# Kernel tuning notes

Hardware: AMD Instinct MI355X
Metric: run time of the kernel (lower is better)

Reference implementation:

```python
import jax, jax.numpy as jnp
import numpy as np

N_CLASSES = 80
IMAGE_SIZE = 608
IGNORE_THR = 0.5
MAX_BOXES = 128  # fixed-size padded replacement for torch's data-dependent masked_select
BATCH = 8
GRIDS = (19, 38, 76)
ANCHORS_NP = np.array([[10, 13], [16, 30], [33, 23], [30, 61], [62, 45], [59, 119],
                       [116, 90], [156, 198], [373, 326]], dtype=np.float32)


def setup_inputs() -> dict:
    key = jax.random.key(0)
    out = {}
    for i, G in enumerate(GRIDS):
        kf, k1, k2, k3, k4 = jax.random.split(jax.random.fold_in(key, i), 5)
        out[f"feature_map_{i}"] = 0.5 * jax.random.normal(kf, (BATCH, 3 * (5 + N_CLASSES), G, G), jnp.float32)
        xy = jax.random.uniform(k1, (BATCH, G, G, 3, 2), jnp.float32, 0.0, float(IMAGE_SIZE))
        wh = jax.random.uniform(k2, (BATCH, G, G, 3, 2), jnp.float32, 10.0, 300.0)
        obj = jax.random.bernoulli(k3, 0.003, (BATCH, G, G, 3, 1)).astype(jnp.float32)
        cls = jax.nn.one_hot(jax.random.randint(k4, (BATCH, G, G, 3), 0, N_CLASSES), N_CLASSES, dtype=jnp.float32)
        out[f"y_true_{i}"] = jnp.concatenate([xy * obj, wh * obj, obj, cls * obj], axis=-1)
    out["anchors"] = jnp.asarray(ANCHORS_NP)
    return out


def _bce_logits(logits, targets):
    # binary_cross_entropy_with_logits, elementwise, numerically stable
    return jnp.maximum(logits, 0.0) - logits * targets + jax.nn.softplus(-jnp.abs(logits))


def _predict_transform(fm, anchors3):
    B, _, G, _ = fm.shape
    stride = IMAGE_SIZE // G
    attrs = 5 + N_CLASSES
    p = fm.reshape(B, 3 * attrs, G * G).transpose(0, 2, 1).reshape(B, G, G, 3, attrs)
    xy, wh, conf, prob = jnp.split(p, [2, 4, 5], axis=-1)
    gx, gy = jnp.meshgrid(jnp.arange(G), jnp.arange(G))  # 'xy' indexing: gx[i,j]=j, gy[i,j]=i
    offset = jnp.stack([gx, gy], axis=-1).astype(p.dtype)[:, :, None, :]  # [G,G,1,2]
    centers = (jax.nn.sigmoid(xy) + offset) * stride  # [B,G,G,3,2]
    sizes = jnp.exp(wh) * (anchors3 / stride) * stride
    boxes = jnp.concatenate([centers, sizes], axis=-1)  # [B,G,G,3,4]
    return offset, boxes, conf, prob, stride


def _ignore_mask(boxes, y_true):
    # Vectorized version of the per-batch masked_select loop: gather up to
    # MAX_BOXES GT boxes per image via top_k on the object flag, mask padding.
    B = boxes.shape[0]
    flags = y_true[..., 4].reshape(B, -1)          # [B, G*G*3]
    tb = y_true[..., :4].reshape(B, -1, 4)          # [B, G*G*3, 4]
    vals, idx = jax.lax.top_k(flags, MAX_BOXES)     # [B,K]
    sel = jnp.take_along_axis(tb, idx[..., None], axis=1)  # [B,K,4]
    valid = vals > 0.5                              # [B,K]
    pxy = boxes[..., 0:2][..., None, :]             # [B,G,G,3,1,2]
    pwh = boxes[..., 2:4][..., None, :]
    txy = sel[:, None, None, None, :, 0:2]          # [B,1,1,1,K,2]
    twh = sel[:, None, None, None, :, 2:4]
    mins = jnp.maximum(pxy - pwh * 0.5, txy - twh * 0.5)
    maxs = jnp.minimum(pxy + pwh * 0.5, txy + twh * 0.5)
    iwh = jnp.maximum(maxs - mins, 0.0)
    inter = iwh[..., 0] * iwh[..., 1]               # [B,G,G,3,K]
    pa = pwh[..., 0] * pwh[..., 1]
    ta = twh[..., 0] * twh[..., 1]
    iou = inter / (pa + ta - inter + 1e-10)
    iou = jnp.where(valid[:, None, None, None, :], iou, 0.0)
    best = jnp.max(iou, axis=-1)                    # [B,G,G,3]
    return (best <= IGNORE_THR).astype(boxes.dtype)[..., None]  # [B,G,G,3,1]


def _scale_loss(fm, yt, anchors3):
    B = yt.shape[0]
    offset, boxes, conf_logits, prob_logits, stride = _predict_transform(fm, anchors3)
    obj = yt[..., 4:5]
    ign = _ignore_mask(boxes, yt)
    pred_xy = boxes[..., 0:2] / stride - offset
    true_xy = yt[..., 0:2] / stride - offset
    true_tw = yt[..., 2:4] / anchors3
    pred_tw = boxes[..., 2:4] / anchors3
    true_tw = jnp.where(true_tw == 0, 1.0, true_tw)
    pred_tw = jnp.where(pred_tw == 0, 1.0, pred_tw)
    true_tw = jnp.log(jnp.clip(true_tw, 1e-9, 1e9))
    pred_tw = jnp.log(jnp.clip(pred_tw, 1e-9, 1e9))
    box_scale = 2.0 - (yt[..., 2:3] / IMAGE_SIZE) * (yt[..., 3:4] / IMAGE_SIZE)
    xy_loss = jnp.sum(5.0 * obj * box_scale * (pred_xy - true_xy) ** 2) / B
    wh_loss = jnp.sum(5.0 * obj * box_scale * (pred_tw - true_tw) ** 2) / B
    bce = _bce_logits(conf_logits, obj)
    conf = obj * bce + 0.5 * (1.0 - obj) * ign * bce
    focal = jnp.abs(obj - jax.nn.sigmoid(conf_logits)) ** 2  # alpha=1, gamma=2
    conf_loss = jnp.sum(conf * focal) / B
    delta = 0.01
    tgt = (1.0 - delta) * yt[..., 5:] + delta / N_CLASSES
    class_loss = jnp.sum(obj * _bce_logits(prob_logits, tgt)) / B
    return xy_loss, wh_loss, conf_loss, class_loss


def reference(feature_map_0, feature_map_1, feature_map_2, y_true_0, y_true_1, y_true_2, anchors):
    fms = (feature_map_0, feature_map_1, feature_map_2)
    yts = (y_true_0, y_true_1, y_true_2)
    list_anchors = (anchors[6:9], anchors[3:6], anchors[0:3])
    xy = wh = cf = pb = 0.0
    for fm, yt, a3 in zip(fms, yts, list_anchors):
        l_xy, l_wh, l_cf, l_pb = _scale_loss(fm, yt, a3)
        xy = xy + l_xy; wh = wh + l_wh; cf = cf + l_cf; pb = pb + l_pb
    total = xy + wh + cf + pb
    return (total, xy, wh, cf, pb)
```

## Files before the change

kernel.cpp:

```cpp
#include <hip/hip_runtime.h>
#include <math.h>

#define NCLS   80
#define ATTRS  85
#define BATCH  8
#define MAXB   128
#define CHCAP  64

constexpr int G0 = 19, G1 = 38, G2 = 76;
constexpr int S0 = G0 * G0, S1 = G1 * G1, S2 = G2 * G2;
constexpr int NPOS0 = 3 * S0, NPOS1 = 3 * S1, NPOS2 = 3 * S2;
constexpr int NCH0 = (NPOS0 + 255) / 256;
constexpr int NCH1 = (NPOS1 + 255) / 256;
constexpr int NCH2 = (NPOS2 + 255) / 256;
constexpr int CHB1 = NCH0 * BATCH;
constexpr int CHB2 = CHB1 + NCH1 * BATCH;
constexpr int TOTCH = CHB2 + NCH2 * BATCH;
constexpr int BW0 = (NPOS0 + 31) / 32;
constexpr int BW1 = (NPOS1 + 31) / 32;
constexpr int BW2 = (NPOS2 + 31) / 32;
constexpr int BMB0 = 0, BMB1 = BW0 * BATCH, BMB2 = BMB1 + BW1 * BATCH;
#define CPB 128
constexpr int MC0 = (S0 + CPB - 1) / CPB;
constexpr int MC1 = (S1 + CPB - 1) / CPB;
constexpr int MC2 = (S2 + CPB - 1) / CPB;
constexpr int MB0 = BATCH * 3 * MC0, MB1 = BATCH * 3 * MC1, MB2 = BATCH * 3 * MC2;
constexpr int NMAIN = MB0 + MB1 + MB2;

#define OFF_CHUNKCNT 0
#define OFF_CHUNKBOX 4096
#define OFF_BITMAP   (4096 + 737280)
#define OFF_PARTA    (4096 + 737280 + 22912)
#define OFF_PARTC    (4096 + 737280 + 22912 + 11520)

__global__ __launch_bounds__(256) void collectA(
    const float* __restrict__ yt0, const float* __restrict__ yt1, const float* __restrict__ yt2,
    const float* __restrict__ fm0, const float* __restrict__ fm1, const float* __restrict__ fm2,
    const float* __restrict__ anchors,
    float4* __restrict__ chunkbox, int* __restrict__ chunkcnt,
    unsigned* __restrict__ bitmap, float* __restrict__ partA)
{
    int blk = blockIdx.x;
    const float* yt; const float* fm;
    int b, c, npos, s, Sv, G, aoff; float strd;
    if (blk < CHB1)      { int q = blk;        b = q / NCH0; c = q % NCH0; npos = NPOS0; yt = yt0; fm = fm0; s = 0; Sv = S0; G = G0; strd = 32.f; aoff = 12; }
    else if (blk < CHB2) { int q = blk - CHB1; b = q / NCH1; c = q % NCH1; npos = NPOS1; yt = yt1; fm = fm1; s = 1; Sv = S1; G = G1; strd = 16.f; aoff = 6; }
    else                 { int q = blk - CHB2; b = q / NCH2; c = q % NCH2; npos = NPOS2; yt = yt2; fm = fm2; s = 2; Sv = S2; G = G2; strd = 8.f;  aoff = 0; }

    int tid = threadIdx.x, wv = tid >> 6, lane = tid & 63;
    int r = c * 256 + tid;
    bool f = false; size_t off = 0;
    if (r < npos) { off = ((size_t)b * npos + r) * ATTRS; f = (yt[off + 4] > 0.5f); }
    unsigned long long m = __ballot(f);

    __shared__ unsigned long long bal[4];
    __shared__ int pr[CHCAP];
    __shared__ float4 pbox[CHCAP];
    __shared__ float wred[4][3];
    if (lane == 0) bal[wv] = m;
    __syncthreads();

    int nw    = (s == 0) ? BW0 : ((s == 1) ? BW1 : BW2);
    int wbase = ((s == 0) ? BMB0 : ((s == 1) ? BMB1 : BMB2)) + b * nw;
    if (tid < 8) {
        int widx = c * 8 + tid;
        if (widx < nw) {
            unsigned long long bm = bal[tid >> 1];
            bitmap[wbase + widx] = (tid & 1) ? (unsigned)(bm >> 32) : (unsigned)bm;
        }
    }

    int prefix = 0, tot = 0;
    #pragma unroll
    for (int i = 0; i < 4; ++i) { int pc = __popcll(bal[i]); if (i < wv) prefix += pc; tot += pc; }
    int myp = prefix + __popcll(m & ((1ull << lane) - 1ull));

    if (f && myp < CHCAP) {
        float4 v; v.x = yt[off]; v.y = yt[off + 1]; v.z = yt[off + 2]; v.w = yt[off + 3];
        chunkbox[blk * CHCAP + myp] = v;
        pr[myp] = r; pbox[myp] = v;
    }
    if (tid == 0) chunkcnt[blk] = (tot > CHCAP) ? CHCAP : tot;
    __syncthreads();

    int np = (tot > CHCAP) ? CHCAP : tot;
    float axy = 0.f, awh = 0.f, acl = 0.f;
    for (int p = wv; p < np; p += 4) {
        int rp = pr[p]; float4 bx = pbox[p];
        int pos = rp / 3, a = rp - pos * 3;
        size_t fb = ((size_t)(b * 255 + a * 85)) * Sv + pos;
        size_t yb = ((size_t)b * npos + rp) * ATTRS;
        float term;
        {
            float pl  = fm[fb + (size_t)(5 + lane) * Sv];
            float tv  = yt[yb + 5 + lane];
            float tgt = 0.99f * tv + 1.25e-4f;
            term = fmaxf(pl, 0.f) - pl * tgt + __logf(1.f + __expf(-fabsf(pl)));
        }
        if (lane < 16) {
            int cc = 64 + lane;
            float pl  = fm[fb + (size_t)(5 + cc) * Sv];
            float tv  = yt[yb + 5 + cc];
            float tgt = 0.99f * tv + 1.25e-4f;
            term += fmaxf(pl, 0.f) - pl * tgt + __logf(1.f + __expf(-fabsf(pl)));
        }
        #pragma unroll
        for (int o = 32; o > 0; o >>= 1) term += __shfl_down(term, o);
        if (lane == 0) {
            float tx = fm[fb];
            float ty = fm[fb + (size_t)Sv];
            float tw = fm[fb + 2 * (size_t)Sv];
            float th = fm[fb + 3 * (size_t)Sv];
            int yr = pos / G, xc = pos - yr * G;
            float sx = 1.f / (1.f + __expf(-tx));
            float sy = 1.f / (1.f + __expf(-ty));
            float predx = (sx + (float)xc) - (float)xc;
            float predy = (sy + (float)yr) - (float)yr;
            float truex = bx.x / strd - (float)xc;
            float truey = bx.y / strd - (float)yr;
            float bs = 2.f - (bx.z / 608.f) * (bx.w / 608.f);
            float dx = predx - truex, dy = predy - truey;
            axy += 5.f * bs * (dx * dx + dy * dy);
            float aw = anchors[aoff + a * 2], ah = anchors[aoff + a * 2 + 1];
            float ttw = __logf(bx.z / aw), tth = __logf(bx.w / ah);
            float dw = tw - ttw, dh = th - tth;
            awh += 5.f * bs * (dw * dw + dh * dh);
            acl += term;
        }
    }
    if (lane == 0) { wred[wv][0] = axy; wred[wv][1] = awh; wred[wv][2] = acl; }
    __syncthreads();
    if (tid == 0) {
        partA[blk * 4 + 0] = wred[0][0] + wred[1][0] + wred[2][0] + wred[3][0];
        partA[blk * 4 + 1] = wred[0][1] + wred[1][1] + wred[2][1] + wred[3][1];
        partA[blk * 4 + 2] = wred[0][2] + wred[1][2] + wred[2][2] + wred[3][2];
        partA[blk * 4 + 3] = 0.f;
    }
}

__global__ __launch_bounds__(128) void conf_final_k(
    const float* __restrict__ fm0, const float* __restrict__ fm1, const float* __restrict__ fm2,
    const float* __restrict__ anchors,
    const float4* __restrict__ chunkbox, const int* __restrict__ chunkcnt,
    const unsigned* __restrict__ bitmap,
    const float4* __restrict__ partA, float* __restrict__ partC,
    float* __restrict__ out)
{
    int blk = blockIdx.x, tid = threadIdx.x;
    int wv = tid >> 6, lane = tid & 63;

    if (blk < NMAIN) {
        int s, q, nchk, G, Sv, aoff; const float* fm; float strd;
        if (blk < MB0)            { s = 0; q = blk;             nchk = MC0; G = G0; Sv = S0; fm = fm0; strd = 32.f; aoff = 12; }
        else if (blk < MB0 + MB1) { s = 1; q = blk - MB0;       nchk = MC1; G = G1; Sv = S1; fm = fm1; strd = 16.f; aoff = 6; }
        else                      { s = 2; q = blk - MB0 - MB1; nchk = MC2; G = G2; Sv = S2; fm = fm2; strd = 8.f;  aoff = 0; }
        int b = q / (3 * nchk); int rem = q % (3 * nchk); int a = rem / nchk; int c = rem % nchk;

        __shared__ float4 sbox[MAXB];
        __shared__ int    cs[130], ps[130];
        __shared__ int    tot_s;
        __shared__ float  sred[2];

        int pos = c * CPB + tid;
        int vld = (pos < Sv);
        size_t fb = ((size_t)(b * 255 + a * 85)) * Sv + (vld ? pos : 0);
        float tx = fm[fb];
        float ty = fm[fb + (size_t)Sv];
        float tw = fm[fb + 2 * (size_t)Sv];
        float th = fm[fb + 3 * (size_t)Sv];
        float tc = fm[fb + 4 * (size_t)Sv];

        int base = (s == 0) ? (b * NCH0) : ((s == 1) ? (CHB1 + b * NCH1) : (CHB2 + b * NCH2));
        int nch  = (s == 0) ? NCH0 : ((s == 1) ? NCH1 : NCH2);
        cs[tid] = (tid < nch) ? chunkcnt[base + tid] : 0;
        __syncthreads();

        if (wv == 0) {
            int c0 = cs[2 * lane], c1 = cs[2 * lane + 1];
            int v = c0 + c1;
            #pragma unroll
            for (int o = 1; o < 64; o <<= 1) {
                int t = __shfl_up(v, o);
                if (lane >= o) v += t;
            }
            int excl = v - (c0 + c1);
            ps[2 * lane]     = excl;
            ps[2 * lane + 1] = excl + c0;
            if (lane == 63) tot_s = v;
        }
        __syncthreads();
        int tot = tot_s;
        int cnt = (tot > MAXB) ? MAXB : tot;

        if (tid < cnt) {
            int lo = 0, hi = nch - 1;
            while (lo < hi) {
                int mid = (lo + hi + 1) >> 1;
                if (ps[mid] <= tid) lo = mid; else hi = mid - 1;
            }
            int j = tid - ps[lo];
            float4 v = chunkbox[(size_t)(base + lo) * CHCAP + j];
            float hw = 0.5f * v.z, hh = 0.5f * v.w;
            sbox[tid] = make_float4(v.x - hw, v.y - hh, v.x + hw, v.y + hh);
        }
        __syncthreads();

        float acc = 0.f;
        if (vld) {
            float aw = anchors[aoff + a * 2], ah = anchors[aoff + a * 2 + 1];
            int yr = pos / G, xc = pos - yr * G;
            float sxg = 1.f / (1.f + __expf(-tx));
            float syg = 1.f / (1.f + __expf(-ty));
            float cx = (sxg + (float)xc) * strd;
            float cy = (syg + (float)yr) * strd;
            float pw = __expf(tw) * aw;
            float ph = __expf(th) * ah;

            int rr = pos * 3 + a;
            int nw    = (s == 0) ? BW0 : ((s == 1) ? BW1 : BW2);
            int wbase = ((s == 0) ? BMB0 : ((s == 1) ? BMB1 : BMB2)) + b * nw;
            unsigned wd = bitmap[wbase + (rr >> 5)];
            float obj = ((wd >> (rr & 31)) & 1u) ? 1.f : 0.f;

            float pa = pw * ph;
            float px0 = cx - 0.5f * pw, py0 = cy - 0.5f * ph;
            float px1 = cx + 0.5f * pw, py1 = cy + 0.5f * ph;
            float best = -1.f;
            for (int j = 0; j < cnt; ++j) {
                float4 bb = sbox[j];
                float ix0 = fmaxf(px0, bb.x);
                float iy0 = fmaxf(py0, bb.y);
                float ix1 = fminf(px1, bb.z);
                float iy1 = fminf(py1, bb.w);
                float iw = fmaxf(ix1 - ix0, 0.f);
                float ih = fmaxf(iy1 - iy0, 0.f);
                float ta = (bb.z - bb.x) * (bb.w - bb.y);
                best = fmaxf(best, 3.f * (iw * ih) - (pa + ta));
            }
            float ign = (best <= 0.f) ? 1.f : 0.f;

            float e    = __expf(-fabsf(tc));
            float l1pe = __logf(1.f + e);
            float bce  = fmaxf(tc, 0.f) - tc * obj + l1pe;
            float sg   = (tc >= 0.f) ? (1.f / (1.f + e)) : (e / (1.f + e));
            float df   = fabsf(obj - sg);
            acc = (obj * bce + 0.5f * (1.f - obj) * ign * bce) * (df * df);
        }

        #pragma unroll
        for (int o = 32; o > 0; o >>= 1) acc += __shfl_down(acc, o);
        if (lane == 0) sred[wv] = acc;
        __syncthreads();
        if (tid == 0) {
            __hip_atomic_store(&partC[blk], sred[0] + sred[1],
                               __ATOMIC_RELAXED, __HIP_MEMORY_SCOPE_AGENT);
        }
    } else {
        float xy = 0.f, wh = 0.f, cl = 0.f;
        for (int i = tid; i < TOTCH; i += 128) {
            float4 v = partA[i];
            xy += v.x; wh += v.y; cl += v.z;
        }
        float cf = 0.f;
        for (int i = tid; i < NMAIN; i += 128) {
            float v; int it = 0;
            do {
                v = __hip_atomic_load(&partC[i], __ATOMIC_RELAXED, __HIP_MEMORY_SCOPE_AGENT);
                if (v > 0.f) break;
                __builtin_amdgcn_s_sleep(2);
            } while (++it < (1 << 18));
            cf += (v > 0.f) ? v : 0.f;
        }
        #pragma unroll
        for (int o = 32; o > 0; o >>= 1) {
            xy += __shfl_down(xy, o);
            wh += __shfl_down(wh, o);
            cl += __shfl_down(cl, o);
            cf += __shfl_down(cf, o);
        }
        __shared__ float red[2][4];
        if (lane == 0) { red[wv][0] = xy; red[wv][1] = wh; red[wv][2] = cl; red[wv][3] = cf; }
        __syncthreads();
        if (tid == 0) {
            float X = (red[0][0] + red[1][0]) * 0.125f;
            float W = (red[0][1] + red[1][1]) * 0.125f;
            float P = (red[0][2] + red[1][2]) * 0.125f;
            float C = (red[0][3] + red[1][3]) * 0.125f;
            out[0] = X + W + C + P;
            out[1] = X; out[2] = W; out[3] = C; out[4] = P;
        }
    }
}

extern "C" void kernel_launch(void* const* d_in, const int* in_sizes, int n_in,
                              void* d_out, int out_size, void* d_ws, size_t ws_size,
                              hipStream_t stream) {
    const float* fm0 = (const float*)d_in[0];
    const float* yt0 = (const float*)d_in[1];
    const float* fm1 = (const float*)d_in[2];
    const float* yt1 = (const float*)d_in[3];
    const float* fm2 = (const float*)d_in[4];
    const float* yt2 = (const float*)d_in[5];
    const float* anch = (const float*)d_in[6];

    char* ws = (char*)d_ws;
    int*      chunkcnt = (int*)(ws + OFF_CHUNKCNT);
    float4*   chunkbox = (float4*)(ws + OFF_CHUNKBOX);
    unsigned* bitmap   = (unsigned*)(ws + OFF_BITMAP);
    float*    partA    = (float*)(ws + OFF_PARTA);
    float*    partC    = (float*)(ws + OFF_PARTC);

    collectA<<<TOTCH, 256, 0, stream>>>(yt0, yt1, yt2, fm0, fm1, fm2, anch,
                                        chunkbox, chunkcnt, bitmap, partA);
    conf_final_k<<<NMAIN + 1, 128, 0, stream>>>(fm0, fm1, fm2, anch,
                                                chunkbox, chunkcnt, bitmap,
                                                (const float4*)partA, partC, (float*)d_out);
}
```

Measured before the change: 23.29 us.

## Fuse collect and conf kernels into one launch with flag-based inter-block polling

Result: slower. 83.46 us (+258.3%).

```diff
diff --git a/kernel.cpp b/kernel.cpp
--- a/kernel.cpp
+++ b/kernel.cpp
@@ -6,6 +6,7 @@
 #define BATCH  8
 #define MAXB   128
 #define CHCAP  64
+#define POLL_TIMEOUT (1 << 18)
 
 constexpr int G0 = 19, G1 = 38, G2 = 76;
 constexpr int S0 = G0 * G0, S1 = G1 * G1, S2 = G2 * G2;
@@ -20,12 +21,10 @@
 constexpr int BW1 = (NPOS1 + 31) / 32;
 constexpr int BW2 = (NPOS2 + 31) / 32;
 constexpr int BMB0 = 0, BMB1 = BW0 * BATCH, BMB2 = BMB1 + BW1 * BATCH;
-#define CPB 128
-constexpr int MC0 = (S0 + CPB - 1) / CPB;
-constexpr int MC1 = (S1 + CPB - 1) / CPB;
-constexpr int MC2 = (S2 + CPB - 1) / CPB;
+constexpr int MC0 = (S0 + 255) / 256, MC1 = (S1 + 255) / 256, MC2 = (S2 + 255) / 256;
 constexpr int MB0 = BATCH * 3 * MC0, MB1 = BATCH * 3 * MC1, MB2 = BATCH * 3 * MC2;
 constexpr int NMAIN = MB0 + MB1 + MB2;
+constexpr int NBLK_TOT = TOTCH + NMAIN + 1;
 
 #define OFF_CHUNKCNT 0
 #define OFF_CHUNKBOX 4096
@@ -33,135 +32,131 @@
 #define OFF_PARTA    (4096 + 737280 + 22912)
 #define OFF_PARTC    (4096 + 737280 + 22912 + 11520)
 
-__global__ __launch_bounds__(256) void collectA(
+__global__ __launch_bounds__(256, 6) void fused_k(
     const float* __restrict__ yt0, const float* __restrict__ yt1, const float* __restrict__ yt2,
     const float* __restrict__ fm0, const float* __restrict__ fm1, const float* __restrict__ fm2,
     const float* __restrict__ anchors,
     float4* __restrict__ chunkbox, int* __restrict__ chunkcnt,
-    unsigned* __restrict__ bitmap, float* __restrict__ partA)
-{
-    int blk = blockIdx.x;
-    const float* yt; const float* fm;
-    int b, c, npos, s, Sv, G, aoff; float strd;
-    if (blk < CHB1)      { int q = blk;        b = q / NCH0; c = q % NCH0; npos = NPOS0; yt = yt0; fm = fm0; s = 0; Sv = S0; G = G0; strd = 32.f; aoff = 12; }
-    else if (blk < CHB2) { int q = blk - CHB1; b = q / NCH1; c = q % NCH1; npos = NPOS1; yt = yt1; fm = fm1; s = 1; Sv = S1; G = G1; strd = 16.f; aoff = 6; }
-    else                 { int q = blk - CHB2; b = q / NCH2; c = q % NCH2; npos = NPOS2; yt = yt2; fm = fm2; s = 2; Sv = S2; G = G2; strd = 8.f;  aoff = 0; }
-
-    int tid = threadIdx.x, wv = tid >> 6, lane = tid & 63;
-    int r = c * 256 + tid;
-    bool f = false; size_t off = 0;
-    if (r < npos) { off = ((size_t)b * npos + r) * ATTRS; f = (yt[off + 4] > 0.5f); }
-    unsigned long long m = __ballot(f);
-
-    __shared__ unsigned long long bal[4];
-    __shared__ int pr[CHCAP];
-    __shared__ float4 pbox[CHCAP];
-    __shared__ float wred[4][3];
-    if (lane == 0) bal[wv] = m;
-    __syncthreads();
-
-    int nw    = (s == 0) ? BW0 : ((s == 1) ? BW1 : BW2);
-    int wbase = ((s == 0) ? BMB0 : ((s == 1) ? BMB1 : BMB2)) + b * nw;
-    if (tid < 8) {
-        int widx = c * 8 + tid;
-        if (widx < nw) {
-            unsigned long long bm = bal[tid >> 1];
-            bitmap[wbase + widx] = (tid & 1) ? (unsigned)(bm >> 32) : (unsigned)bm;
-        }
-    }
-
-    int prefix = 0, tot = 0;
-    #pragma unroll
-    for (int i = 0; i < 4; ++i) { int pc = __popcll(bal[i]); if (i < wv) prefix += pc; tot += pc; }
-    int myp = prefix + __popcll(m & ((1ull << lane) - 1ull));
-
-    if (f && myp < CHCAP) {
-        float4 v; v.x = yt[off]; v.y = yt[off + 1]; v.z = yt[off + 2]; v.w = yt[off + 3];
-        chunkbox[blk * CHCAP + myp] = v;
-        pr[myp] = r; pbox[myp] = v;
-    }
-    if (tid == 0) chunkcnt[blk] = (tot > CHCAP) ? CHCAP : tot;
-    __syncthreads();
-
-    int np = (tot > CHCAP) ? CHCAP : tot;
-    float axy = 0.f, awh = 0.f, acl = 0.f;
-    for (int p = wv; p < np; p += 4) {
-        int rp = pr[p]; float4 bx = pbox[p];
-        int pos = rp / 3, a = rp - pos * 3;
-        size_t fb = ((size_t)(b * 255 + a * 85)) * Sv + pos;
-        size_t yb = ((size_t)b * npos + rp) * ATTRS;
-        float term;
-        {
-            float pl  = fm[fb + (size_t)(5 + lane) * Sv];
-            float tv  = yt[yb + 5 + lane];
-            float tgt = 0.99f * tv + 1.25e-4f;
-            term = fmaxf(pl, 0.f) - pl * tgt + __logf(1.f + __expf(-fabsf(pl)));
-        }
-        if (lane < 16) {
-            int cc = 64 + lane;
-            float pl  = fm[fb + (size_t)(5 + cc) * Sv];
-            float tv  = yt[yb + 5 + cc];
-            float tgt = 0.99f * tv + 1.25e-4f;
-            term += fmaxf(pl, 0.f) - pl * tgt + __logf(1.f + __expf(-fabsf(pl)));
-        }
-        #pragma unroll
-        for (int o = 32; o > 0; o >>= 1) term += __shfl_down(term, o);
-        if (lane == 0) {
-            float tx = fm[fb];
-            float ty = fm[fb + (size_t)Sv];
-            float tw = fm[fb + 2 * (size_t)Sv];
-            float th = fm[fb + 3 * (size_t)Sv];
-            int yr = pos / G, xc = pos - yr * G;
-            float sx = 1.f / (1.f + __expf(-tx));
-            float sy = 1.f / (1.f + __expf(-ty));
-            float predx = (sx + (float)xc) - (float)xc;
-            float predy = (sy + (float)yr) - (float)yr;
-            float truex = bx.x / strd - (float)xc;
-            float truey = bx.y / strd - (float)yr;
-            float bs = 2.f - (bx.z / 608.f) * (bx.w / 608.f);
-            float dx = predx - truex, dy = predy - truey;
-            axy += 5.f * bs * (dx * dx + dy * dy);
-            float aw = anchors[aoff + a * 2], ah = anchors[aoff + a * 2 + 1];
-            float ttw = __logf(bx.z / aw), tth = __logf(bx.w / ah);
-            float dw = tw - ttw, dh = th - tth;
-            awh += 5.f * bs * (dw * dw + dh * dh);
-            acl += term;
-        }
-    }
-    if (lane == 0) { wred[wv][0] = axy; wred[wv][1] = awh; wred[wv][2] = acl; }
-    __syncthreads();
-    if (tid == 0) {
-        partA[blk * 4 + 0] = wred[0][0] + wred[1][0] + wred[2][0] + wred[3][0];
-        partA[blk * 4 + 1] = wred[0][1] + wred[1][1] + wred[2][1] + wred[3][1];
-        partA[blk * 4 + 2] = wred[0][2] + wred[1][2] + wred[2][2] + wred[3][2];
-        partA[blk * 4 + 3] = 0.f;
-    }
-}
-
-__global__ __launch_bounds__(128) void conf_final_k(
-    const float* __restrict__ fm0, const float* __restrict__ fm1, const float* __restrict__ fm2,
-    const float* __restrict__ anchors,
-    const float4* __restrict__ chunkbox, const int* __restrict__ chunkcnt,
-    const unsigned* __restrict__ bitmap,
-    const float4* __restrict__ partA, float* __restrict__ partC,
+    unsigned* __restrict__ bitmap,
+    float* __restrict__ partA, float* __restrict__ partC,
     float* __restrict__ out)
 {
-    int blk = blockIdx.x, tid = threadIdx.x;
-    int wv = tid >> 6, lane = tid & 63;
-
-    if (blk < NMAIN) {
+    int blk = blockIdx.x, tid = threadIdx.x, wv = tid >> 6, lane = tid & 63;
+
+    if (blk < TOTCH) {
+        const float* yt; const float* fm;
+        int b, c, npos, s, Sv, G, aoff; float strd;
+        if (blk < CHB1)      { int q = blk;        b = q / NCH0; c = q % NCH0; npos = NPOS0; yt = yt0; fm = fm0; s = 0; Sv = S0; G = G0; strd = 32.f; aoff = 12; }
+        else if (blk < CHB2) { int q = blk - CHB1; b = q / NCH1; c = q % NCH1; npos = NPOS1; yt = yt1; fm = fm1; s = 1; Sv = S1; G = G1; strd = 16.f; aoff = 6; }
+        else                 { int q = blk - CHB2; b = q / NCH2; c = q % NCH2; npos = NPOS2; yt = yt2; fm = fm2; s = 2; Sv = S2; G = G2; strd = 8.f;  aoff = 0; }
+
+        int r = c * 256 + tid;
+        bool f = false; size_t off = 0;
+        if (r < npos) { off = ((size_t)b * npos + r) * ATTRS; f = (yt[off + 4] > 0.5f); }
+        unsigned long long m = __ballot(f);
+
+        __shared__ unsigned long long bal[4];
+        __shared__ int pr[CHCAP];
+        __shared__ float4 pbox[CHCAP];
+        __shared__ float wred[4][3];
+        if (lane == 0) bal[wv] = m;
+        __syncthreads();
+
+        int nw    = (s == 0) ? BW0 : ((s == 1) ? BW1 : BW2);
+        int wbase = ((s == 0) ? BMB0 : ((s == 1) ? BMB1 : BMB2)) + b * nw;
+        if (tid < 8) {
+            int widx = c * 8 + tid;
+            if (widx < nw) {
+                unsigned long long bm = bal[tid >> 1];
+                bitmap[wbase + widx] = (tid & 1) ? (unsigned)(bm >> 32) : (unsigned)bm;
+            }
+        }
+
+        int prefix = 0, tot = 0;
+        #pragma unroll
+        for (int i = 0; i < 4; ++i) { int pc = __popcll(bal[i]); if (i < wv) prefix += pc; tot += pc; }
+        int myp = prefix + __popcll(m & ((1ull << lane) - 1ull));
+
+        if (f && myp < CHCAP) {
+            float4 v; v.x = yt[off]; v.y = yt[off + 1]; v.z = yt[off + 2]; v.w = yt[off + 3];
+            chunkbox[blk * CHCAP + myp] = v;
+            pr[myp] = r; pbox[myp] = v;
+        }
+        __syncthreads();
+
+        int np = (tot > CHCAP) ? CHCAP : tot;
+        if (tid == 0) {
+            __hip_atomic_store(&chunkcnt[blk], np + 1, __ATOMIC_RELEASE, __HIP_MEMORY_SCOPE_AGENT);
+        }
+
+        float axy = 0.f, awh = 0.f, acl = 0.f;
+        for (int p = wv; p < np; p += 4) {
+            int rp = pr[p]; float4 bx = pbox[p];
+            int pos = rp / 3, a = rp - pos * 3;
+            size_t fb = ((size_t)(b * 255 + a * 85)) * Sv + pos;
+            size_t yb = ((size_t)b * npos + rp) * ATTRS;
+            float term;
+            {
+                float pl  = fm[fb + (size_t)(5 + lane) * Sv];
+                float tv  = yt[yb + 5 + lane];
+                float tgt = 0.99f * tv + 1.25e-4f;
+                term = fmaxf(pl, 0.f) - pl * tgt + __logf(1.f + __expf(-fabsf(pl)));
+            }
+            if (lane < 16) {
+                int cc = 64 + lane;
+                float pl  = fm[fb + (size_t)(5 + cc) * Sv];
+                float tv  = yt[yb + 5 + cc];
+                float tgt = 0.99f * tv + 1.25e-4f;
+                term += fmaxf(pl, 0.f) - pl * tgt + __logf(1.f + __expf(-fabsf(pl)));
+            }
+            #pragma unroll
+            for (int o = 32; o > 0; o >>= 1) term += __shfl_down(term, o);
+            if (lane == 0) {
+                float tx = fm[fb];
+                float ty = fm[fb + (size_t)Sv];
+                float tw = fm[fb + 2 * (size_t)Sv];
+                float th = fm[fb + 3 * (size_t)Sv];
+                int yr = pos / G, xc = pos - yr * G;
+                float sx = 1.f / (1.f + __expf(-tx));
+                float sy = 1.f / (1.f + __expf(-ty));
+                float predx = (sx + (float)xc) - (float)xc;
+                float predy = (sy + (float)yr) - (float)yr;
+                float truex = bx.x / strd - (float)xc;
+                float truey = bx.y / strd - (float)yr;
+                float bs = 2.f - (bx.z / 608.f) * (bx.w / 608.f);
+                float dx = predx - truex, dy = predy - truey;
+                axy += 5.f * bs * (dx * dx + dy * dy);
+                float aw = anchors[aoff + a * 2], ah = anchors[aoff + a * 2 + 1];
+                float ttw = __logf(bx.z / aw), tth = __logf(bx.w / ah);
+                float dw = tw - ttw, dh = th - tth;
+                awh += 5.f * bs * (dw * dw + dh * dh);
+                acl += term;
+            }
+        }
+        if (lane == 0) { wred[wv][0] = axy; wred[wv][1] = awh; wred[wv][2] = acl; }
+        __syncthreads();
+        if (tid == 0) {
+            float4* pav = (float4*)partA;
+            pav[blk] = make_float4(wred[0][0] + wred[1][0] + wred[2][0] + wred[3][0],
+                                   wred[0][1] + wred[1][1] + wred[2][1] + wred[3][1],
+                                   wred[0][2] + wred[1][2] + wred[2][2] + wred[3][2], 0.f);
+            __hip_atomic_store(&partA[blk * 4 + 3], 1.0f, __ATOMIC_RELEASE, __HIP_MEMORY_SCOPE_AGENT);
+        }
+
+    } else if (blk < TOTCH + NMAIN) {
+        int u = blk - TOTCH;
         int s, q, nchk, G, Sv, aoff; const float* fm; float strd;
-        if (blk < MB0)            { s = 0; q = blk;             nchk = MC0; G = G0; Sv = S0; fm = fm0; strd = 32.f; aoff = 12; }
-        else if (blk < MB0 + MB1) { s = 1; q = blk - MB0;       nchk = MC1; G = G1; Sv = S1; fm = fm1; strd = 16.f; aoff = 6; }
-        else                      { s = 2; q = blk - MB0 - MB1; nchk = MC2; G = G2; Sv = S2; fm = fm2; strd = 8.f;  aoff = 0; }
+        if (u < MB0)            { s = 0; q = u;             nchk = MC0; G = G0; Sv = S0; fm = fm0; strd = 32.f; aoff = 12; }
+        else if (u < MB0 + MB1) { s = 1; q = u - MB0;       nchk = MC1; G = G1; Sv = S1; fm = fm1; strd = 16.f; aoff = 6; }
+        else                    { s = 2; q = u - MB0 - MB1; nchk = MC2; G = G2; Sv = S2; fm = fm2; strd = 8.f;  aoff = 0; }
         int b = q / (3 * nchk); int rem = q % (3 * nchk); int a = rem / nchk; int c = rem % nchk;
 
         __shared__ float4 sbox[MAXB];
         __shared__ int    cs[130], ps[130];
         __shared__ int    tot_s;
-        __shared__ float  sred[2];
-
-        int pos = c * CPB + tid;
+        __shared__ float  sred[4];
+
+        int pos = c * 256 + tid;
         int vld = (pos < Sv);
         size_t fb = ((size_t)(b * 255 + a * 85)) * Sv + (vld ? pos : 0);
         float tx = fm[fb];
@@ -172,8 +167,20 @@
 
         int base = (s == 0) ? (b * NCH0) : ((s == 1) ? (CHB1 + b * NCH1) : (CHB2 + b * NCH2));
         int nch  = (s == 0) ? NCH0 : ((s == 1) ? NCH1 : NCH2);
-        cs[tid] = (tid < nch) ? chunkcnt[base + tid] : 0;
-        __syncthreads();
+        if (tid < 128) {
+            int v1 = 0;
+            if (tid < nch) {
+                int it = 0;
+                do {
+                    v1 = __hip_atomic_load(&chunkcnt[base + tid], __ATOMIC_RELAXED, __HIP_MEMORY_SCOPE_AGENT);
+                    if (v1 > 0) break;
+                    __builtin_amdgcn_s_sleep(2);
+                } while (++it < POLL_TIMEOUT);
+            }
+            cs[tid] = (v1 > 0) ? (v1 - 1) : 0;
+        }
+        __syncthreads();
+        __threadfence();
 
         if (wv == 0) {
             int c0 = cs[2 * lane], c1 = cs[2 * lane + 1];
@@ -252,23 +259,36 @@
         if (lane == 0) sred[wv] = acc;
         __syncthreads();
         if (tid == 0) {
-            __hip_atomic_store(&partC[blk], sred[0] + sred[1],
+            __hip_atomic_store(&partC[u], sred[0] + sred[1] + sred[2] + sred[3],
                                __ATOMIC_RELAXED, __HIP_MEMORY_SCOPE_AGENT);
         }
+
     } else {
+        for (int i = tid; i < TOTCH; i += 256) {
+            int it = 0;
+            while (it < POLL_TIMEOUT) {
+                float v = __hip_atomic_load(&partA[i * 4 + 3], __ATOMIC_RELAXED, __HIP_MEMORY_SCOPE_AGENT);
+                if (v == 1.0f) break;
+                __builtin_amdgcn_s_sleep(2);
+                ++it;
+            }
+        }
+        __syncthreads();
+        __threadfence();
         float xy = 0.f, wh = 0.f, cl = 0.f;
-        for (int i = tid; i < TOTCH; i += 128) {
-            float4 v = partA[i];
+        const float4* pav = (const float4*)partA;
+        for (int i = tid; i < TOTCH; i += 256) {
+            float4 v = pav[i];
             xy += v.x; wh += v.y; cl += v.z;
         }
         float cf = 0.f;
-        for (int i = tid; i < NMAIN; i += 128) {
+        for (int i = tid; i < NMAIN; i += 256) {
             float v; int it = 0;
             do {
                 v = __hip_atomic_load(&partC[i], __ATOMIC_RELAXED, __HIP_MEMORY_SCOPE_AGENT);
                 if (v > 0.f) break;
                 __builtin_amdgcn_s_sleep(2);
-            } while (++it < (1 << 18));
+            } while (++it < POLL_TIMEOUT);
             cf += (v > 0.f) ? v : 0.f;
         }
         #pragma unroll
@@ -278,14 +298,14 @@
             cl += __shfl_down(cl, o);
             cf += __shfl_down(cf, o);
         }
-        __shared__ float red[2][4];
+        __shared__ float red[4][4];
         if (lane == 0) { red[wv][0] = xy; red[wv][1] = wh; red[wv][2] = cl; red[wv][3] = cf; }
         __syncthreads();
         if (tid == 0) {
-            float X = (red[0][0] + red[1][0]) * 0.125f;
-            float W = (red[0][1] + red[1][1]) * 0.125f;
-            float P = (red[0][2] + red[1][2]) * 0.125f;
-            float C = (red[0][3] + red[1][3]) * 0.125f;
+            float X = (red[0][0] + red[1][0] + red[2][0] + red[3][0]) * 0.125f;
+            float W = (red[0][1] + red[1][1] + red[2][1] + red[3][1]) * 0.125f;
+            float P = (red[0][2] + red[1][2] + red[2][2] + red[3][2]) * 0.125f;
+            float C = (red[0][3] + red[1][3] + red[2][3] + red[3][3]) * 0.125f;
             out[0] = X + W + C + P;
             out[1] = X; out[2] = W; out[3] = C; out[4] = P;
         }
@@ -310,9 +330,7 @@
     float*    partA    = (float*)(ws + OFF_PARTA);
     float*    partC    = (float*)(ws + OFF_PARTC);
 
-    collectA<<<TOTCH, 256, 0, stream>>>(yt0, yt1, yt2, fm0, fm1, fm2, anch,
-                                        chunkbox, chunkcnt, bitmap, partA);
-    conf_final_k<<<NMAIN + 1, 128, 0, stream>>>(fm0, fm1, fm2, anch,
-                                                chunkbox, chunkcnt, bitmap,
-                                                (const float4*)partA, partC, (float*)d_out);
+    fused_k<<<NBLK_TOT, 256, 0, stream>>>(yt0, yt1, yt2, fm0, fm1, fm2, anch,
+                                          chunkbox, chunkcnt, bitmap,
+                                          partA, partC, (float*)d_out);
 }
```

## Move positive-box loss work from collect kernel into second kernel blocks

Applied to the files above, without the earlier changes.

Result: slower. 31.03 us (+33.2%).

```diff
diff --git a/kernel.cpp b/kernel.cpp
--- a/kernel.cpp
+++ b/kernel.cpp
@@ -6,6 +6,7 @@
 #define BATCH  8
 #define MAXB   128
 #define CHCAP  64
+#define POLL_TIMEOUT (1 << 18)
 
 constexpr int G0 = 19, G1 = 38, G2 = 76;
 constexpr int S0 = G0 * G0, S1 = G1 * G1, S2 = G2 * G2;
@@ -26,26 +27,26 @@
 constexpr int MC2 = (S2 + CPB - 1) / CPB;
 constexpr int MB0 = BATCH * 3 * MC0, MB1 = BATCH * 3 * MC1, MB2 = BATCH * 3 * MC2;
 constexpr int NMAIN = MB0 + MB1 + MB2;
+constexpr int NBLK2 = NMAIN + TOTCH + 1;
 
 #define OFF_CHUNKCNT 0
 #define OFF_CHUNKBOX 4096
-#define OFF_BITMAP   (4096 + 737280)
-#define OFF_PARTA    (4096 + 737280 + 22912)
-#define OFF_PARTC    (4096 + 737280 + 22912 + 11520)
+#define OFF_CHUNKIDX (4096 + 737280)
+#define OFF_BITMAP   (4096 + 737280 + 184320)
+#define OFF_PARTA    (4096 + 737280 + 184320 + 22912)
+#define OFF_PARTC    (4096 + 737280 + 184320 + 22912 + 11520)
 
 __global__ __launch_bounds__(256) void collectA(
     const float* __restrict__ yt0, const float* __restrict__ yt1, const float* __restrict__ yt2,
-    const float* __restrict__ fm0, const float* __restrict__ fm1, const float* __restrict__ fm2,
-    const float* __restrict__ anchors,
-    float4* __restrict__ chunkbox, int* __restrict__ chunkcnt,
-    unsigned* __restrict__ bitmap, float* __restrict__ partA)
+    float4* __restrict__ chunkbox, int* __restrict__ chunkidx, int* __restrict__ chunkcnt,
+    unsigned* __restrict__ bitmap)
 {
     int blk = blockIdx.x;
-    const float* yt; const float* fm;
-    int b, c, npos, s, Sv, G, aoff; float strd;
-    if (blk < CHB1)      { int q = blk;        b = q / NCH0; c = q % NCH0; npos = NPOS0; yt = yt0; fm = fm0; s = 0; Sv = S0; G = G0; strd = 32.f; aoff = 12; }
-    else if (blk < CHB2) { int q = blk - CHB1; b = q / NCH1; c = q % NCH1; npos = NPOS1; yt = yt1; fm = fm1; s = 1; Sv = S1; G = G1; strd = 16.f; aoff = 6; }
-    else                 { int q = blk - CHB2; b = q / NCH2; c = q % NCH2; npos = NPOS2; yt = yt2; fm = fm2; s = 2; Sv = S2; G = G2; strd = 8.f;  aoff = 0; }
+    const float* yt;
+    int b, c, npos, s;
+    if (blk < CHB1)      { int q = blk;        b = q / NCH0; c = q % NCH0; npos = NPOS0; yt = yt0; s = 0; }
+    else if (blk < CHB2) { int q = blk - CHB1; b = q / NCH1; c = q % NCH1; npos = NPOS1; yt = yt1; s = 1; }
+    else                 { int q = blk - CHB2; b = q / NCH2; c = q % NCH2; npos = NPOS2; yt = yt2; s = 2; }
 
     int tid = threadIdx.x, wv = tid >> 6, lane = tid & 63;
     int r = c * 256 + tid;
@@ -54,9 +55,6 @@
     unsigned long long m = __ballot(f);
 
     __shared__ unsigned long long bal[4];
-    __shared__ int pr[CHCAP];
-    __shared__ float4 pbox[CHCAP];
-    __shared__ float wred[4][3];
     if (lane == 0) bal[wv] = m;
     __syncthreads();
 
@@ -77,77 +75,22 @@
 
     if (f && myp < CHCAP) {
         float4 v; v.x = yt[off]; v.y = yt[off + 1]; v.z = yt[off + 2]; v.w = yt[off + 3];
-        chunkbox[blk * CHCAP + myp] = v;
-        pr[myp] = r; pbox[myp] = v;
+        chunkbox[(size_t)blk * CHCAP + myp] = v;
+        chunkidx[blk * CHCAP + myp] = r;
     }
     if (tid == 0) chunkcnt[blk] = (tot > CHCAP) ? CHCAP : tot;
-    __syncthreads();
-
-    int np = (tot > CHCAP) ? CHCAP : tot;
-    float axy = 0.f, awh = 0.f, acl = 0.f;
-    for (int p = wv; p < np; p += 4) {
-        int rp = pr[p]; float4 bx = pbox[p];
-        int pos = rp / 3, a = rp - pos * 3;
-        size_t fb = ((size_t)(b * 255 + a * 85)) * Sv + pos;
-        size_t yb = ((size_t)b * npos + rp) * ATTRS;
-        float term;
-        {
-            float pl  = fm[fb + (size_t)(5 + lane) * Sv];
-            float tv  = yt[yb + 5 + lane];
-            float tgt = 0.99f * tv + 1.25e-4f;
-            term = fmaxf(pl, 0.f) - pl * tgt + __logf(1.f + __expf(-fabsf(pl)));
-        }
-        if (lane < 16) {
-            int cc = 64 + lane;
-            float pl  = fm[fb + (size_t)(5 + cc) * Sv];
-            float tv  = yt[yb + 5 + cc];
-            float tgt = 0.99f * tv + 1.25e-4f;
-            term += fmaxf(pl, 0.f) - pl * tgt + __logf(1.f + __expf(-fabsf(pl)));
-        }
-        #pragma unroll
-        for (int o = 32; o > 0; o >>= 1) term += __shfl_down(term, o);
-        if (lane == 0) {
-            float tx = fm[fb];
-            float ty = fm[fb + (size_t)Sv];
-            float tw = fm[fb + 2 * (size_t)Sv];
-            float th = fm[fb + 3 * (size_t)Sv];
-            int yr = pos / G, xc = pos - yr * G;
-            float sx = 1.f / (1.f + __expf(-tx));
-            float sy = 1.f / (1.f + __expf(-ty));
-            float predx = (sx + (float)xc) - (float)xc;
-            float predy = (sy + (float)yr) - (float)yr;
-            float truex = bx.x / strd - (float)xc;
-            float truey = bx.y / strd - (float)yr;
-            float bs = 2.f - (bx.z / 608.f) * (bx.w / 608.f);
-            float dx = predx - truex, dy = predy - truey;
-            axy += 5.f * bs * (dx * dx + dy * dy);
-            float aw = anchors[aoff + a * 2], ah = anchors[aoff + a * 2 + 1];
-            float ttw = __logf(bx.z / aw), tth = __logf(bx.w / ah);
-            float dw = tw - ttw, dh = th - tth;
-            awh += 5.f * bs * (dw * dw + dh * dh);
-            acl += term;
-        }
-    }
-    if (lane == 0) { wred[wv][0] = axy; wred[wv][1] = awh; wred[wv][2] = acl; }
-    __syncthreads();
-    if (tid == 0) {
-        partA[blk * 4 + 0] = wred[0][0] + wred[1][0] + wred[2][0] + wred[3][0];
-        partA[blk * 4 + 1] = wred[0][1] + wred[1][1] + wred[2][1] + wred[3][1];
-        partA[blk * 4 + 2] = wred[0][2] + wred[1][2] + wred[2][2] + wred[3][2];
-        partA[blk * 4 + 3] = 0.f;
-    }
 }
 
-__global__ __launch_bounds__(128) void conf_final_k(
+__global__ __launch_bounds__(128) void work_k(
+    const float* __restrict__ yt0, const float* __restrict__ yt1, const float* __restrict__ yt2,
     const float* __restrict__ fm0, const float* __restrict__ fm1, const float* __restrict__ fm2,
     const float* __restrict__ anchors,
-    const float4* __restrict__ chunkbox, const int* __restrict__ chunkcnt,
-    const unsigned* __restrict__ bitmap,
-    const float4* __restrict__ partA, float* __restrict__ partC,
+    const float4* __restrict__ chunkbox, const int* __restrict__ chunkidx,
+    const int* __restrict__ chunkcnt, const unsigned* __restrict__ bitmap,
+    float* __restrict__ partA, float* __restrict__ partC,
     float* __restrict__ out)
 {
-    int blk = blockIdx.x, tid = threadIdx.x;
-    int wv = tid >> 6, lane = tid & 63;
+    int blk = blockIdx.x, tid = threadIdx.x, wv = tid >> 6, lane = tid & 63;
 
     if (blk < NMAIN) {
         int s, q, nchk, G, Sv, aoff; const float* fm; float strd;
@@ -255,10 +198,96 @@
             __hip_atomic_store(&partC[blk], sred[0] + sred[1],
                                __ATOMIC_RELAXED, __HIP_MEMORY_SCOPE_AGENT);
         }
+
+    } else if (blk < NMAIN + TOTCH) {
+        int u2 = blk - NMAIN;
+        const float* yt; const float* fm;
+        int b, npos, s, Sv, G, aoff; float strd;
+        if (u2 < CHB1)      { int q = u2;        b = q / NCH0; npos = NPOS0; yt = yt0; fm = fm0; s = 0; Sv = S0; G = G0; strd = 32.f; aoff = 12; }
+        else if (u2 < CHB2) { int q = u2 - CHB1; b = q / NCH1; npos = NPOS1; yt = yt1; fm = fm1; s = 1; Sv = S1; G = G1; strd = 16.f; aoff = 6; }
+        else                { int q = u2 - CHB2; b = q / NCH2; npos = NPOS2; yt = yt2; fm = fm2; s = 2; Sv = S2; G = G2; strd = 8.f;  aoff = 0; }
+
+        __shared__ int    pr[CHCAP];
+        __shared__ float4 pbox[CHCAP];
+        __shared__ float  wred[2][3];
+
+        int np = chunkcnt[u2];
+        if (tid < np) {
+            pr[tid]   = chunkidx[u2 * CHCAP + tid];
+            pbox[tid] = chunkbox[(size_t)u2 * CHCAP + tid];
+        }
+        __syncthreads();
+
+        float axy = 0.f, awh = 0.f, acl = 0.f;
+        for (int p = wv; p < np; p += 2) {
+            int rp = pr[p]; float4 bx = pbox[p];
+            int pos = rp / 3, a = rp - pos * 3;
+            size_t fb = ((size_t)(b * 255 + a * 85)) * Sv + pos;
+            size_t yb = ((size_t)b * npos + rp) * ATTRS;
+            float term;
+            {
+                float pl  = fm[fb + (size_t)(5 + lane) * Sv];
+                float tv  = yt[yb + 5 + lane];
+                float tgt = 0.99f * tv + 1.25e-4f;
+                term = fmaxf(pl, 0.f) - pl * tgt + __logf(1.f + __expf(-fabsf(pl)));
+            }
+            if (lane < 16) {
+                int cc = 64 + lane;
+                float pl  = fm[fb + (size_t)(5 + cc) * Sv];
+                float tv  = yt[yb + 5 + cc];
+                float tgt = 0.99f * tv + 1.25e-4f;
+                term += fmaxf(pl, 0.f) - pl * tgt + __logf(1.f + __expf(-fabsf(pl)));
+            }
+            #pragma unroll
+            for (int o = 32; o > 0; o >>= 1) term += __shfl_down(term, o);
+            if (lane == 0) {
+                float tx = fm[fb];
+                float ty = fm[fb + (size_t)Sv];
+                float tw = fm[fb + 2 * (size_t)Sv];
+                float th = fm[fb + 3 * (size_t)Sv];
+                int yr = pos / G, xc = pos - yr * G;
+                float sx = 1.f / (1.f + __expf(-tx));
+                float sy = 1.f / (1.f + __expf(-ty));
+                float predx = (sx + (float)xc) - (float)xc;
+                float predy = (sy + (float)yr) - (float)yr;
+                float truex = bx.x / strd - (float)xc;
+                float truey = bx.y / strd - (float)yr;
+                float bs = 2.f - (bx.z / 608.f) * (bx.w / 608.f);
+                float dx = predx - truex, dy = predy - truey;
+                axy += 5.f * bs * (dx * dx + dy * dy);
+                float aw = anchors[aoff + a * 2], ah = anchors[aoff + a * 2 + 1];
+                float ttw = __logf(bx.z / aw), tth = __logf(bx.w / ah);
+                float dw = tw - ttw, dh = th - tth;
+                awh += 5.f * bs * (dw * dw + dh * dh);
+                acl += term;
+            }
+        }
+        if (lane == 0) { wred[wv][0] = axy; wred[wv][1] = awh; wred[wv][2] = acl; }
+        __syncthreads();
+        if (tid == 0) {
+            float4* pav = (float4*)partA;
+            pav[u2] = make_float4(wred[0][0] + wred[1][0],
+                                  wred[0][1] + wred[1][1],
+                                  wred[0][2] + wred[1][2], 0.f);
+            __hip_atomic_store(&partA[u2 * 4 + 3], 1.0f, __ATOMIC_RELEASE, __HIP_MEMORY_SCOPE_AGENT);
+        }
+
     } else {
+        for (int i = tid; i < TOTCH; i += 128) {
+            int it = 0;
+            while (it < POLL_TIMEOUT) {
+                float v = __hip_atomic_load(&partA[i * 4 + 3], __ATOMIC_RELAXED, __HIP_MEMORY_SCOPE_AGENT);
+                if (v == 1.0f) break;
+                __builtin_amdgcn_s_sleep(2);
+                ++it;
+            }
+        }
+        __syncthreads();
+        __threadfence();
         float xy = 0.f, wh = 0.f, cl = 0.f;
+        const float4* pav = (const float4*)partA;
         for (int i = tid; i < TOTCH; i += 128) {
-            float4 v = partA[i];
+            float4 v = pav[i];
             xy += v.x; wh += v.y; cl += v.z;
         }
         float cf = 0.f;
@@ -268,7 +297,7 @@
                 v = __hip_atomic_load(&partC[i], __ATOMIC_RELAXED, __HIP_MEMORY_SCOPE_AGENT);
                 if (v > 0.f) break;
                 __builtin_amdgcn_s_sleep(2);
-            } while (++it < (1 << 18));
+            } while (++it < POLL_TIMEOUT);
             cf += (v > 0.f) ? v : 0.f;
         }
         #pragma unroll
@@ -306,13 +335,13 @@
     char* ws = (char*)d_ws;
     int*      chunkcnt = (int*)(ws + OFF_CHUNKCNT);
     float4*   chunkbox = (float4*)(ws + OFF_CHUNKBOX);
+    int*      chunkidx = (int*)(ws + OFF_CHUNKIDX);
     unsigned* bitmap   = (unsigned*)(ws + OFF_BITMAP);
     float*    partA    = (float*)(ws + OFF_PARTA);
     float*    partC    = (float*)(ws + OFF_PARTC);
 
-    collectA<<<TOTCH, 256, 0, stream>>>(yt0, yt1, yt2, fm0, fm1, fm2, anch,
-                                        chunkbox, chunkcnt, bitmap, partA);
-    conf_final_k<<<NMAIN + 1, 128, 0, stream>>>(fm0, fm1, fm2, anch,
-                                                chunkbox, chunkcnt, bitmap,
-                                                (const float4*)partA, partC, (float*)d_out);
+    collectA<<<TOTCH, 256, 0, stream>>>(yt0, yt1, yt2, chunkbox, chunkidx, chunkcnt, bitmap);
+    work_k<<<NBLK2, 128, 0, stream>>>(yt0, yt1, yt2, fm0, fm1, fm2, anch,
+                                      chunkbox, chunkidx, chunkcnt, bitmap,
+                                      partA, partC, (float*)d_out);
 }
```
